# Kernel optimization log

Measured on AMD Instinct MI355X. Metric: run time of the kernel, lower is better.

The kernel has to match this reference:

```python
import jax, jax.numpy as jnp
import numpy as np

D_MODEL = 1024
N_HEADS = 16
D_HEAD = D_MODEL // N_HEADS
D_FF = 4096
EPS = 1e-5


def layer_norm(x, g, b):
    mu = jnp.mean(x, axis=-1, keepdims=True)
    var = jnp.mean(jnp.square(x - mu), axis=-1, keepdims=True)
    return (x - mu) * jax.lax.rsqrt(var + EPS) * g + b


def setup_inputs() -> dict:
    key = jax.random.key(0)
    ks = jax.random.split(key, 8)
    s = 1.0 / np.sqrt(D_MODEL)
    return {
        "x": jax.random.normal(ks[0], (2, 2048, D_MODEL), dtype=jnp.float32),
        "Wq": jax.random.normal(ks[1], (N_HEADS, D_MODEL, D_HEAD), dtype=jnp.float32) * s,
        "Wk": jax.random.normal(ks[2], (N_HEADS, D_MODEL, D_HEAD), dtype=jnp.float32) * s,
        "Wv": jax.random.normal(ks[3], (N_HEADS, D_MODEL, D_HEAD), dtype=jnp.float32) * s,
        "Wo": jax.random.normal(ks[4], (D_MODEL, D_MODEL), dtype=jnp.float32) * s,
        "bo": jnp.zeros((D_MODEL,), dtype=jnp.float32),
        "ln1_g": jnp.ones((D_MODEL,), dtype=jnp.float32),
        "ln1_b": jnp.zeros((D_MODEL,), dtype=jnp.float32),
        "ln2_g": jnp.ones((D_MODEL,), dtype=jnp.float32),
        "ln2_b": jnp.zeros((D_MODEL,), dtype=jnp.float32),
        "W1": jax.random.normal(ks[5], (D_MODEL, D_FF), dtype=jnp.float32) * s,
        "b1": jnp.zeros((D_FF,), dtype=jnp.float32),
        "W2": jax.random.normal(ks[6], (D_FF, D_MODEL), dtype=jnp.float32) * (1.0 / np.sqrt(D_FF)),
        "b2": jnp.zeros((D_MODEL,), dtype=jnp.float32),
    }


def reference(x, Wq, Wk, Wv, Wo, bo, ln1_g, ln1_b, ln2_g, ln2_b, W1, b1, W2, b2):
    # Pre-norm MHA (per-head projections batched over head axis h)
    xn = layer_norm(x, ln1_g, ln1_b)
    q = jnp.einsum("bsd,hde->bhse", xn, Wq)
    k = jnp.einsum("bsd,hde->bhse", xn, Wk)
    v = jnp.einsum("bsd,hde->bhse", xn, Wv)
    scores = jnp.einsum("bhqe,bhke->bhqk", q, k) / jnp.sqrt(jnp.float32(D_HEAD))
    w = jax.nn.softmax(scores, axis=-1)
    attn = jnp.einsum("bhqk,bhke->bhqe", w, v)  # [b,h,s,dh]
    b, h, s, dh = attn.shape
    concat = attn.transpose(0, 2, 1, 3).reshape(b, s, h * dh)  # head concat order matches torch cat
    attn_out = concat @ Wo + bo
    hidden = x + attn_out
    hn = layer_norm(hidden, ln2_g, ln2_b)
    ff = jax.nn.gelu(hn @ W1 + b1, approximate=False) @ W2 + b2  # torch nn.GELU default = exact
    return hidden + ff
```

## Files before the change

kernel.cpp:

```cpp
#include <hip/hip_runtime.h>
#include <hip/hip_bf16.h>

typedef __bf16 bf16;
typedef __bf16 bf16x4 __attribute__((ext_vector_type(4)));
typedef __bf16 bf16x8 __attribute__((ext_vector_type(8)));
typedef float  f32x4  __attribute__((ext_vector_type(4)));

static __device__ __forceinline__ f32x4 mfma16(bf16x8 a, bf16x8 b, f32x4 c) {
  return __builtin_amdgcn_mfma_f32_16x16x32_bf16(a, b, c, 0, 0, 0);
}

static __device__ __forceinline__ float fexp2(float x) {
  return __builtin_amdgcn_exp2f(x);
}

static __device__ __forceinline__ void gl_lds16(const bf16* g, bf16* l) {
  __builtin_amdgcn_global_load_lds(
      (const __attribute__((address_space(1))) void*)g,
      (__attribute__((address_space(3))) void*)l, 16, 0, 0);
}

struct TrTab {
  const float* src[6];
  bf16* dst[6];
  int R[6], C[6], ntx[6], nty[6];
  int base[7];
};

__global__ __launch_bounds__(256) void tr6_kernel(TrTab tab) {
  int bid = blockIdx.x;
  int j = 0;
  while (j < 5 && bid >= tab.base[j + 1]) ++j;
  const int local = bid - tab.base[j];
  const int R = tab.R[j], C = tab.C[j];
  const int ntx = tab.ntx[j];
  const int per_z = ntx * tab.nty[j];
  const int z = local / per_z;
  const int rem = local - z * per_z;
  const int by = rem / ntx, bx = rem - by * ntx;
  const float* in = tab.src[j];
  bf16* out = tab.dst[j];

  __shared__ bf16 tile[32][33];
  const size_t zoff = (size_t)z * R * C;
  const int tx = threadIdx.x & 31, ty = threadIdx.x >> 5;
  const int x = bx * 32 + tx;
  const int y0 = by * 32;
#pragma unroll
  for (int jj = 0; jj < 4; ++jj)
    tile[ty + jj * 8][tx] = (bf16)in[zoff + (size_t)(y0 + ty + jj * 8) * C + x];
  __syncthreads();
  const int x2 = y0 + tx;
  const int y2 = bx * 32;
#pragma unroll
  for (int jj = 0; jj < 4; ++jj)
    out[zoff + (size_t)(y2 + ty + jj * 8) * R + x2] = tile[tx][ty + jj * 8];
}

__global__ __launch_bounds__(256) void trb_kernel(const bf16* __restrict__ inp,
                                                  bf16* __restrict__ out,
                                                  int R, int C) {
  __shared__ bf16 tile[32][33];
  const size_t zoff = (size_t)blockIdx.z * R * C;
  const int tx = threadIdx.x & 31, ty = threadIdx.x >> 5;
  const int x = blockIdx.x * 32 + tx;
  const int y0 = blockIdx.y * 32;
#pragma unroll
  for (int j = 0; j < 4; ++j)
    tile[ty + j * 8][tx] = inp[zoff + (size_t)(y0 + ty + j * 8) * C + x];
  __syncthreads();
  const int x2 = y0 + tx;
  const int y2 = blockIdx.x * 32;
#pragma unroll
  for (int j = 0; j < 4; ++j)
    out[zoff + (size_t)(y2 + ty + j * 8) * R + x2] = tile[tx][ty + j * 8];
}

__global__ __launch_bounds__(256) void ln_kernel(const float* __restrict__ inp,
                                                 const float* __restrict__ g,
                                                 const float* __restrict__ bt,
                                                 bf16* __restrict__ outp) {
  const int row = blockIdx.x;
  const int t = threadIdx.x;
  f32x4 v = ((const f32x4*)inp)[row * 256 + t];
  float s = v[0] + v[1] + v[2] + v[3];
  float sq = v[0] * v[0] + v[1] * v[1] + v[2] * v[2] + v[3] * v[3];
#pragma unroll
  for (int off = 32; off > 0; off >>= 1) {
    s += __shfl_xor(s, off);
    sq += __shfl_xor(sq, off);
  }
  __shared__ float red[8];
  const int wave = t >> 6, lane = t & 63;
  if (lane == 0) {
    red[wave] = s;
    red[wave + 4] = sq;
  }
  __syncthreads();
  s = red[0] + red[1] + red[2] + red[3];
  sq = red[4] + red[5] + red[6] + red[7];
  const float mu = s * (1.0f / 1024.0f);
  const float var = sq * (1.0f / 1024.0f) - mu * mu;
  const float rstd = rsqrtf(fmaxf(var, 0.0f) + 1e-5f);
  f32x4 gg = ((const f32x4*)g)[t];
  f32x4 bb = ((const f32x4*)bt)[t];
  bf16 o[4];
#pragma unroll
  for (int i = 0; i < 4; ++i)
    o[i] = (bf16)((v[i] - mu) * rstd * gg[i] + bb[i]);
  *(uint2*)&outp[(size_t)row * 1024 + 4 * t] = *(uint2*)o;
}

enum { EPI_QKV = 0, EPI_O = 1, EPI_FF1 = 2, EPI_FF2 = 3 };

template <int EPI, bool NARROW>
__global__ __launch_bounds__(256) void gemm_bt(
    const bf16* __restrict__ A, const bf16* __restrict__ Bt, const int K,
    const float* __restrict__ bias, const float* __restrict__ res,
    bf16* __restrict__ outB, float* __restrict__ outF) {
  constexpr int BN = NARROW ? 64 : 128;
  constexpr int NI = NARROW ? 2 : 4;
  constexpr int BCH = BN / 32;
  __shared__ __align__(16) bf16 sA[2][128 * 64];
  __shared__ __align__(16) bf16 sB[2][BN * 64];
  const int t = threadIdx.x;
  const int lane = t & 63, wave = t >> 6;
  const int quad = lane >> 4, l15 = lane & 15;
  const int wr = wave >> 1, wc = wave & 1;
  const int m0 = blockIdx.y * 128, n0 = blockIdx.x * BN;
  const int srow = lane >> 3;
  const int scol = ((lane & 7) ^ srow) * 8;

  const bf16* aPtr[4];
#pragma unroll
  for (int c = 0; c < 4; ++c)
    aPtr[c] = A + (size_t)(m0 + wave * 32 + c * 8 + srow) * K + scol;
  const bf16* bPtr[BCH];
#pragma unroll
  for (int c = 0; c < BCH; ++c)
    bPtr[c] = Bt + (size_t)(n0 + wave * (BCH * 8) + c * 8 + srow) * K + scol;

  f32x4 acc[4][NI];
#pragma unroll
  for (int i = 0; i < 4; ++i)
#pragma unroll
    for (int j = 0; j < NI; ++j) acc[i][j] = {0.f, 0.f, 0.f, 0.f};

  const int niter = K >> 6;
#pragma unroll
  for (int c = 0; c < 4; ++c)
    gl_lds16(aPtr[c], &sA[0][(wave * 4 + c) * 512]);
#pragma unroll
  for (int c = 0; c < BCH; ++c)
    gl_lds16(bPtr[c], &sB[0][(wave * BCH + c) * 512]);

  for (int it = 0; it < niter; ++it) {
    const int cur = it & 1, nxt = cur ^ 1;
    __syncthreads();
    if (it + 1 < niter) {
      const int off = (it + 1) * 64;
#pragma unroll
      for (int c = 0; c < 4; ++c)
        gl_lds16(aPtr[c] + off, &sA[nxt][(wave * 4 + c) * 512]);
#pragma unroll
      for (int c = 0; c < BCH; ++c)
        gl_lds16(bPtr[c] + off, &sB[nxt][(wave * BCH + c) * 512]);
    }
#pragma unroll
    for (int ks = 0; ks < 2; ++ks) {
      bf16x8 af[4], bfr[NI];
#pragma unroll
      for (int mi = 0; mi < 4; ++mi) {
        const int row = wr * 64 + mi * 16 + l15;
        const int col = ((ks * 4 + quad) ^ (row & 7)) * 8;
        af[mi] = *(const bf16x8*)&sA[cur][row * 64 + col];
      }
#pragma unroll
      for (int ni = 0; ni < NI; ++ni) {
        const int row = wc * (BN / 2) + ni * 16 + l15;
        const int col = ((ks * 4 + quad) ^ (row & 7)) * 8;
        bfr[ni] = *(const bf16x8*)&sB[cur][row * 64 + col];
      }
#pragma unroll
      for (int mi = 0; mi < 4; ++mi)
#pragma unroll
        for (int ni = 0; ni < NI; ++ni)
          acc[mi][ni] = mfma16(af[mi], bfr[ni], acc[mi][ni]);
    }
  }

#pragma unroll
  for (int mi = 0; mi < 4; ++mi) {
#pragma unroll
    for (int ni = 0; ni < NI; ++ni) {
      const int n = n0 + wc * (BN / 2) + ni * 16 + l15;
#pragma unroll
      for (int r = 0; r < 4; ++r) {
        const int m = m0 + wr * 64 + mi * 16 + quad * 4 + r;
        float v = acc[mi][ni][r];
        if constexpr (EPI == EPI_QKV) {
          const int which = n >> 10, nn = n & 1023;
          const int h = nn >> 6, e = nn & 63;
          const int b = m >> 11, s2 = m & 2047;
          outB[(size_t)which * 4194304 +
               ((size_t)(b * 16 + h) * 2048 + s2) * 64 + e] = (bf16)v;
        } else if constexpr (EPI == EPI_O) {
          v += bias[n] + res[(size_t)m * 1024 + n];
          outF[(size_t)m * 1024 + n] = v;
        } else if constexpr (EPI == EPI_FF1) {
          v += bias[n];
          v = 0.5f * v * (1.0f + erff(v * 0.70710678118654752f));
          outB[(size_t)m * 4096 + n] = (bf16)v;
        } else {
          v += bias[n] + res[(size_t)m * 1024 + n];
          outF[(size_t)m * 1024 + n] = v;
        }
      }
    }
  }
}

__global__ __launch_bounds__(512, 4) void attn_kernel(
    const bf16* __restrict__ q, const bf16* __restrict__ k,
    const bf16* __restrict__ vt, bf16* __restrict__ ao) {
  __shared__ __align__(16) bf16 sP[256 * 72];
  __shared__ __align__(16) bf16 sK[2][64 * 64];
  __shared__ __align__(16) bf16 sV[2][64 * 64];
  const int t = threadIdx.x;
  const int lane = t & 63, wave = t >> 6;
  const int wq = wave & 3, kh = wave >> 2;
  const int quad = lane >> 4, l15 = lane & 15;
  const int q0 = blockIdx.x * 128;
  const int bh = blockIdx.y, b = bh >> 4, h = bh & 15;
  const bf16* Q  = q  + (size_t)bh * 2048 * 64;
  const bf16* Kp = k  + (size_t)bh * 2048 * 64 + (size_t)kh * 1024 * 64;
  const bf16* Vt = vt + (size_t)bh * 64 * 2048 + kh * 1024;
  const int srow = lane >> 3;
  const int scol = ((lane & 7) ^ srow) * 8;
  const float SCL = 0.125f * 1.4426950408889634f;

#pragma unroll
  for (int c = 0; c < 2; ++c) {
    const int chunk = wave * 2 + c;
    const int row = chunk * 8 + srow;
    gl_lds16(&Q[(size_t)(q0 + row) * 64 + scol], &sP[chunk * 512]);
  }
  __syncthreads();
  bf16x8 qf[2][2];
#pragma unroll
  for (int mi = 0; mi < 2; ++mi)
#pragma unroll
    for (int ks = 0; ks < 2; ++ks) {
      const int row = wq * 32 + mi * 16 + l15;
      const int col = ((ks * 4 + quad) ^ (row & 7)) * 8;
      qf[mi][ks] = *(const bf16x8*)&sP[row * 64 + col];
    }
  __syncthreads();

  f32x4 o[2][4];
  float ls[2] = {0.f, 0.f};
#pragma unroll
  for (int mi = 0; mi < 2; ++mi)
#pragma unroll
    for (int ne = 0; ne < 4; ++ne) o[mi][ne] = {0.f, 0.f, 0.f, 0.f};

  for (int kb = 0; kb < 16; ++kb) {
    const int kbase = kb * 64;
    __syncthreads();
#pragma unroll
    for (int c = 0; c < 2; ++c) {
      const int chunk = wq * 2 + c;
      const int row = chunk * 8 + srow;
      gl_lds16(&Kp[(size_t)(kbase + row) * 64 + scol], &sK[kh][chunk * 512]);
      gl_lds16(&Vt[(size_t)row * 2048 + kbase + scol], &sV[kh][chunk * 512]);
    }
    __syncthreads();

    f32x4 s[4][2];
#pragma unroll
    for (int ni = 0; ni < 4; ++ni)
#pragma unroll
      for (int mi = 0; mi < 2; ++mi) s[ni][mi] = {0.f, 0.f, 0.f, 0.f};
#pragma unroll
    for (int ks = 0; ks < 2; ++ks) {
      bf16x8 kf[4];
#pragma unroll
      for (int ni = 0; ni < 4; ++ni) {
        const int row = ni * 16 + l15;
        const int col = ((ks * 4 + quad) ^ (row & 7)) * 8;
        kf[ni] = *(const bf16x8*)&sK[kh][row * 64 + col];
      }
#pragma unroll
      for (int ni = 0; ni < 4; ++ni)
#pragma unroll
        for (int mi = 0; mi < 2; ++mi)
          s[ni][mi] = mfma16(kf[ni], qf[mi][ks], s[ni][mi]);
    }

#pragma unroll
    for (int mi = 0; mi < 2; ++mi)
#pragma unroll
      for (int ni = 0; ni < 4; ++ni) {
        bf16x4 p4;
#pragma unroll
        for (int r = 0; r < 4; ++r) {
          const float p = fexp2(s[ni][mi][r] * SCL);
          ls[mi] += p;
          p4[r] = (bf16)p;
        }
        *(bf16x4*)&sP[(wave * 32 + mi * 16 + l15) * 72 + ni * 16 + quad * 4] =
            p4;
      }

#pragma unroll
    for (int ksb = 0; ksb < 2; ++ksb) {
      bf16x8 vf[4];
#pragma unroll
      for (int ne = 0; ne < 4; ++ne) {
        const int row = ne * 16 + l15;
        const int col = ((ksb * 4 + quad) ^ (row & 7)) * 8;
        vf[ne] = *(const bf16x8*)&sV[kh][row * 64 + col];
      }
#pragma unroll
      for (int mi = 0; mi < 2; ++mi) {
        const bf16x8 pf = *(const bf16x8*)&sP[(wave * 32 + mi * 16 + l15) * 72 +
                                              ksb * 32 + quad * 8];
#pragma unroll
        for (int ne = 0; ne < 4; ++ne)
          o[mi][ne] = mfma16(pf, vf[ne], o[mi][ne]);
      }
    }
  }

#pragma unroll
  for (int mi = 0; mi < 2; ++mi) {
    ls[mi] += __shfl_xor(ls[mi], 16);
    ls[mi] += __shfl_xor(ls[mi], 32);
  }

  float* mo = (float*)sP;
  float* ml = (float*)sK;
  __syncthreads();
  if (kh == 1) {
    const int base = (wq * 64 + lane) * 32;
#pragma unroll
    for (int mi = 0; mi < 2; ++mi)
#pragma unroll
      for (int ne = 0; ne < 4; ++ne)
        *(f32x4*)&mo[base + (mi * 4 + ne) * 4] = o[mi][ne];
    ml[(wq * 64 + lane) * 2 + 0] = ls[0];
    ml[(wq * 64 + lane) * 2 + 1] = ls[1];
  }
  __syncthreads();
  if (kh == 0) {
    const int base = (wq * 64 + lane) * 32;
#pragma unroll
    for (int mi = 0; mi < 2; ++mi) {
#pragma unroll
      for (int ne = 0; ne < 4; ++ne) {
        const f32x4 add = *(const f32x4*)&mo[base + (mi * 4 + ne) * 4];
#pragma unroll
        for (int r = 0; r < 4; ++r) o[mi][ne][r] += add[r];
      }
      ls[mi] += ml[(wq * 64 + lane) * 2 + mi];
      ls[mi] = 1.0f / fmaxf(ls[mi], 1e-30f);
    }
#pragma unroll
    for (int mi = 0; mi < 2; ++mi) {
      float linv[4];
#pragma unroll
      for (int r = 0; r < 4; ++r) linv[r] = __shfl(ls[mi], quad * 4 + r);
#pragma unroll
      for (int ne = 0; ne < 4; ++ne)
#pragma unroll
        for (int r = 0; r < 4; ++r) {
          const int row = q0 + wq * 32 + mi * 16 + quad * 4 + r;
          const int col = h * 64 + ne * 16 + l15;
          ao[((size_t)(b * 2048 + row)) * 1024 + col] =
              (bf16)(o[mi][ne][r] * linv[r]);
        }
    }
  }
}

extern "C" void kernel_launch(void* const* d_in, const int* in_sizes, int n_in,
                              void* d_out, int out_size, void* d_ws,
                              size_t ws_size, hipStream_t stream) {
  const float* x    = (const float*)d_in[0];
  const float* Wq   = (const float*)d_in[1];
  const float* Wk   = (const float*)d_in[2];
  const float* Wv   = (const float*)d_in[3];
  const float* Wo   = (const float*)d_in[4];
  const float* bo   = (const float*)d_in[5];
  const float* ln1g = (const float*)d_in[6];
  const float* ln1b = (const float*)d_in[7];
  const float* ln2g = (const float*)d_in[8];
  const float* ln2b = (const float*)d_in[9];
  const float* W1   = (const float*)d_in[10];
  const float* b1   = (const float*)d_in[11];
  const float* W2   = (const float*)d_in[12];
  const float* b2   = (const float*)d_in[13];

  char* ws = (char*)d_ws;
  const size_t MB = 1ull << 20;
  bf16* QKVT = (bf16*)(ws);
  bf16* WqT  = QKVT;
  bf16* WkT  = (bf16*)(ws + 2 * MB);
  bf16* WvT  = (bf16*)(ws + 4 * MB);
  bf16* WoT  = (bf16*)(ws + 6 * MB);
  bf16* W1T  = (bf16*)(ws + 8 * MB);
  bf16* W2T  = (bf16*)(ws + 16 * MB);
  bf16* sh8  = (bf16*)(ws + 24 * MB);
  bf16* qb   = (bf16*)(ws + 32 * MB);
  bf16* kb   = (bf16*)(ws + 40 * MB);
  bf16* vb   = (bf16*)(ws + 48 * MB);
  bf16* vtb  = (bf16*)(ws + 56 * MB);
  bf16* h1   = (bf16*)(ws + 32 * MB);
  float* hid = (float*)(ws + 64 * MB);

  const dim3 blk(256);

  TrTab tab;
  const float* srcs[6] = {Wq, Wk, Wv, Wo, W1, W2};
  bf16* dsts[6] = {WqT, WkT, WvT, WoT, W1T, W2T};
  const int Rs[6] = {1024, 1024, 1024, 1024, 1024, 4096};
  const int Cs[6] = {64, 64, 64, 1024, 4096, 1024};
  const int Zs[6] = {16, 16, 16, 1, 1, 1};
  int base = 0;
  for (int j = 0; j < 6; ++j) {
    tab.src[j] = srcs[j];
    tab.dst[j] = dsts[j];
    tab.R[j] = Rs[j];
    tab.C[j] = Cs[j];
    tab.ntx[j] = Cs[j] / 32;
    tab.nty[j] = Rs[j] / 32;
    tab.base[j] = base;
    base += (Cs[j] / 32) * (Rs[j] / 32) * Zs[j];
  }
  tab.base[6] = base;
  tr6_kernel<<<base, blk, 0, stream>>>(tab);

  ln_kernel<<<4096, blk, 0, stream>>>(x, ln1g, ln1b, sh8);
  gemm_bt<EPI_QKV, false><<<dim3(24, 32), blk, 0, stream>>>(
      sh8, QKVT, 1024, nullptr, nullptr, qb, nullptr);
  trb_kernel<<<dim3(2, 64, 32), blk, 0, stream>>>(vb, vtb, 2048, 64);
  attn_kernel<<<dim3(16, 32), dim3(512), 0, stream>>>(qb, kb, vtb, sh8);
  gemm_bt<EPI_O, true><<<dim3(16, 32), blk, 0, stream>>>(
      sh8, WoT, 1024, bo, x, nullptr, hid);
  ln_kernel<<<4096, blk, 0, stream>>>(hid, ln2g, ln2b, sh8);
  gemm_bt<EPI_FF1, false><<<dim3(32, 32), blk, 0, stream>>>(
      sh8, W1T, 1024, b1, nullptr, h1, nullptr);
  gemm_bt<EPI_FF2, true><<<dim3(16, 32), blk, 0, stream>>>(
      h1, W2T, 4096, b2, hid, nullptr, (float*)d_out);

  (void)in_sizes; (void)n_in; (void)out_size; (void)ws_size;
}
```

Measured before the change: 357.6 us.

## Add 256x256-tile 8-wave GEMM with interleaved pipeline for QKV and FF1

```diff
diff --git a/kernel.cpp b/kernel.cpp
--- a/kernel.cpp
+++ b/kernel.cpp
@@ -112,6 +112,173 @@
 }
 
 enum { EPI_QKV = 0, EPI_O = 1, EPI_FF1 = 2, EPI_FF2 = 3 };
+
+#define VMW(N) asm volatile("s_waitcnt vmcnt(" #N ")" ::: "memory")
+#define BARR                        \
+  do {                              \
+    __builtin_amdgcn_s_barrier();   \
+    asm volatile("" ::: "memory");  \
+  } while (0)
+
+template <int EPI>
+__global__ __launch_bounds__(512) void gemm256(
+    const bf16* __restrict__ A, const bf16* __restrict__ Bt, const int K,
+    const float* __restrict__ bias, bf16* __restrict__ outB) {
+  __shared__ __align__(16) bf16 sA[2][256 * 64];
+  __shared__ __align__(16) bf16 sB[2][256 * 64];
+  const int t = threadIdx.x;
+  const int lane = t & 63, wave = t >> 6;
+  const int quad = lane >> 4, l15 = lane & 15;
+  const int wm = wave >> 2, wn = wave & 3;
+  const int m0 = blockIdx.y * 256, n0 = blockIdx.x * 256;
+  const int srow = lane >> 3;
+  const int scol = ((lane & 7) ^ srow) * 8;
+  const int bch = (wave & 3) + (wave >> 2) * 8;
+
+  const bf16* aS0 = A + (size_t)(m0 + wave * 8 + srow) * K + scol;
+  const bf16* aS1 = aS0 + (size_t)64 * K;
+  const bf16* bS0 = Bt + (size_t)(n0 + bch * 8 + srow) * K + scol;
+  const bf16* bS1 = bS0 + (size_t)32 * K;
+  const size_t rsk = (size_t)128 * K;
+
+  auto stA0 = [&](int buf, int ko) {
+    gl_lds16(aS0 + ko, &sA[buf][wave * 512]);
+    gl_lds16(aS0 + ko + rsk, &sA[buf][(wave + 16) * 512]);
+  };
+  auto stB0 = [&](int buf, int ko) {
+    gl_lds16(bS0 + ko, &sB[buf][bch * 512]);
+    gl_lds16(bS0 + ko + rsk, &sB[buf][(bch + 16) * 512]);
+  };
+  auto stB1 = [&](int buf, int ko) {
+    gl_lds16(bS1 + ko, &sB[buf][(bch + 4) * 512]);
+    gl_lds16(bS1 + ko + rsk, &sB[buf][(bch + 20) * 512]);
+  };
+  auto stA1 = [&](int buf, int ko) {
+    gl_lds16(aS1 + ko, &sA[buf][(wave + 8) * 512]);
+    gl_lds16(aS1 + ko + rsk, &sA[buf][(wave + 24) * 512]);
+  };
+
+  f32x4 acc[8][4];
+#pragma unroll
+  for (int i = 0; i < 8; ++i)
+#pragma unroll
+    for (int j = 0; j < 4; ++j) acc[i][j] = {0.f, 0.f, 0.f, 0.f};
+
+  bf16x8 af[4][2], bf0[2][2], bf1[2][2];
+
+  auto ldA = [&](int buf, int mh) {
+#pragma unroll
+    for (int i = 0; i < 4; ++i) {
+      const int row = wm * 128 + mh * 64 + i * 16 + l15;
+#pragma unroll
+      for (int ks = 0; ks < 2; ++ks) {
+        const int col = ((ks * 4 + quad) ^ (row & 7)) * 8;
+        af[i][ks] = *(const bf16x8*)&sA[buf][row * 64 + col];
+      }
+    }
+  };
+  auto ldB = [&](int buf, int nh, bf16x8 (&bfm)[2][2]) {
+#pragma unroll
+    for (int j = 0; j < 2; ++j) {
+      const int row = wn * 64 + nh * 32 + j * 16 + l15;
+#pragma unroll
+      for (int ks = 0; ks < 2; ++ks) {
+        const int col = ((ks * 4 + quad) ^ (row & 7)) * 8;
+        bfm[j][ks] = *(const bf16x8*)&sB[buf][row * 64 + col];
+      }
+    }
+  };
+  auto mm = [&](int mh, int nh, bf16x8 (&bfm)[2][2]) {
+    asm volatile("s_waitcnt lgkmcnt(0)" ::: "memory");
+    __builtin_amdgcn_sched_barrier(0);
+    __builtin_amdgcn_s_setprio(1);
+#pragma unroll
+    for (int ks = 0; ks < 2; ++ks)
+#pragma unroll
+      for (int i = 0; i < 4; ++i)
+#pragma unroll
+        for (int j = 0; j < 2; ++j)
+          acc[mh * 4 + i][nh * 2 + j] =
+              mfma16(af[i][ks], bfm[j][ks], acc[mh * 4 + i][nh * 2 + j]);
+    __builtin_amdgcn_s_setprio(0);
+    __builtin_amdgcn_sched_barrier(0);
+  };
+
+  stA0(0, 0);
+  stB0(0, 0);
+  stB1(0, 0);
+  stA1(0, 0);
+
+  const int NT = K >> 6;
+#pragma unroll 1
+  for (int it = 0; it < NT - 1; ++it) {
+    const int cur = it & 1, nxt = cur ^ 1;
+    const int ko = (it + 1) * 64;
+    VMW(4);
+    BARR;
+    ldA(cur, 0);
+    ldB(cur, 0, bf0);
+    stA0(nxt, ko);
+    mm(0, 0, bf0);
+    VMW(4);
+    BARR;
+    ldB(cur, 1, bf1);
+    stB0(nxt, ko);
+    mm(0, 1, bf1);
+    VMW(4);
+    BARR;
+    ldA(cur, 1);
+    stB1(nxt, ko);
+    mm(1, 1, bf1);
+    ldB(cur, 0, bf0);
+    stA1(nxt, ko);
+    mm(1, 0, bf0);
+  }
+  {
+    const int cur = (NT - 1) & 1;
+    VMW(4);
+    BARR;
+    ldA(cur, 0);
+    ldB(cur, 0, bf0);
+    mm(0, 0, bf0);
+    VMW(2);
+    BARR;
+    ldB(cur, 1, bf1);
+    mm(0, 1, bf1);
+    VMW(0);
+    BARR;
+    ldA(cur, 1);
+    mm(1, 1, bf1);
+    ldB(cur, 0, bf0);
+    mm(1, 0, bf0);
+  }
+
+#pragma unroll
+  for (int ni = 0; ni < 4; ++ni) {
+    const int n = n0 + wn * 64 + ni * 16 + l15;
+    float bv = 0.f;
+    if constexpr (EPI == EPI_FF1) bv = bias[n];
+#pragma unroll
+    for (int mi = 0; mi < 8; ++mi) {
+#pragma unroll
+      for (int r = 0; r < 4; ++r) {
+        const int m = m0 + wm * 128 + mi * 16 + quad * 4 + r;
+        float v = acc[mi][ni][r];
+        if constexpr (EPI == EPI_QKV) {
+          const int which = n >> 10, nn = n & 1023;
+          const int h = nn >> 6, e = nn & 63;
+          const int b = m >> 11, s2 = m & 2047;
+          outB[(size_t)which * 4194304 +
+               ((size_t)(b * 16 + h) * 2048 + s2) * 64 + e] = (bf16)v;
+        } else {
+          v += bv;
+          v = 0.5f * v * (1.0f + erff(v * 0.70710678118654752f));
+          outB[(size_t)m * 4096 + n] = (bf16)v;
+        }
+      }
+    }
+  }
+}
 
 template <int EPI, bool NARROW>
 __global__ __launch_bounds__(256) void gemm_bt(
@@ -441,15 +608,15 @@
   tr6_kernel<<<base, blk, 0, stream>>>(tab);
 
   ln_kernel<<<4096, blk, 0, stream>>>(x, ln1g, ln1b, sh8);
-  gemm_bt<EPI_QKV, false><<<dim3(24, 32), blk, 0, stream>>>(
-      sh8, QKVT, 1024, nullptr, nullptr, qb, nullptr);
+  gemm256<EPI_QKV><<<dim3(12, 16), dim3(512), 0, stream>>>(
+      sh8, QKVT, 1024, nullptr, qb);
   trb_kernel<<<dim3(2, 64, 32), blk, 0, stream>>>(vb, vtb, 2048, 64);
   attn_kernel<<<dim3(16, 32), dim3(512), 0, stream>>>(qb, kb, vtb, sh8);
   gemm_bt<EPI_O, true><<<dim3(16, 32), blk, 0, stream>>>(
       sh8, WoT, 1024, bo, x, nullptr, hid);
   ln_kernel<<<4096, blk, 0, stream>>>(hid, ln2g, ln2b, sh8);
-  gemm_bt<EPI_FF1, false><<<dim3(32, 32), blk, 0, stream>>>(
-      sh8, W1T, 1024, b1, nullptr, h1, nullptr);
+  gemm256<EPI_FF1><<<dim3(16, 16), dim3(512), 0, stream>>>(
+      sh8, W1T, 1024, b1, h1);
   gemm_bt<EPI_FF2, true><<<dim3(16, 32), blk, 0, stream>>>(
       h1, W2T, 4096, b2, hid, nullptr, (float*)d_out);
 
```

Result: no change. 364.1 us (+1.8%).
